# Performance work log

Hardware: AMD Instinct MI355X
Metric: run time of the kernel (lower is better)

## Reference

```python
import jax, jax.numpy as jnp
import numpy as np

LN_EPS = 1e-5


def setup_inputs() -> dict:
    key = jax.random.key(0)
    ks = jax.random.split(key, 10)
    b, n, m, d, e = 2, 4096, 32, 128, 64
    return {
        "t_ij": jax.random.normal(ks[0], (b, n, m, d), dtype=jnp.float32),
        "x1": jax.random.normal(ks[1], (b, n, d, 3), dtype=jnp.float32),
        "x2": jax.random.normal(ks[2], (b, n, d, 5), dtype=jnp.float32),
        "neighbor_indices": jax.random.randint(ks[3], (b, n, m), 0, n),
        "to_queries": jax.random.normal(ks[4], (d, e), dtype=jnp.float32),
        "to_keys1": jax.random.normal(ks[5], (d, e), dtype=jnp.float32),
        "to_keys2": jax.random.normal(ks[6], (d, e), dtype=jnp.float32),
        "ln_weight": jnp.ones((2 * e,), dtype=jnp.float32),
        "edge_w": jax.random.normal(ks[7], (2 * e, d), dtype=jnp.float32) / np.sqrt(2 * e),
        "res_w": jax.random.normal(ks[8], (d, d), dtype=jnp.float32) / np.sqrt(d),
    }


def _degree_inner_product(xl, to_queries, to_keys, neighbor_indices):
    # xl: [b n d ml]; projections over channel dim d -> e
    q = jnp.einsum('bndm,de->bnem', xl, to_queries)   # [b n e ml]
    k = jnp.einsum('bndm,de->bnem', xl, to_keys)      # [b n e ml]
    # gather neighbor keys: [b n j e ml]
    kg = jax.vmap(lambda kk, idx: kk[idx])(k, neighbor_indices)
    # inner product over multiplicity ml, per feature e: [b n j e]
    return jnp.einsum('bnem,bnjem->bnje', q, kg)


def reference(t_ij, x1, x2, neighbor_indices, to_queries, to_keys1, to_keys2,
              ln_weight, edge_w, res_w):
    ip1 = _degree_inner_product(x1, to_queries, to_keys1, neighbor_indices)
    ip2 = _degree_inner_product(x2, to_queries, to_keys2, neighbor_indices)
    w_ij = jnp.concatenate([ip1, ip2], axis=-1)  # [b n j 2e]
    # LayerNorm over last dim, weight only (bias=False)
    mu = jnp.mean(w_ij, axis=-1, keepdims=True)
    var = jnp.mean((w_ij - mu) ** 2, axis=-1, keepdims=True)
    w_ij = (w_ij - mu) * jax.lax.rsqrt(var + LN_EPS) * ln_weight
    edge_out = jax.nn.sigmoid(jnp.einsum('bnje,ed->bnjd', w_ij, edge_w))
    res_out = jnp.einsum('bnjd,de->bnje', t_ij, res_w)
    return edge_out + res_out
```

## Files before the change

kernel.cpp:

```cpp
#include <hip/hip_runtime.h>

#define B_ 2
#define N_ 4096
#define M_ 32
#define D_ 128
#define E_ 64
#define LN_EPS 1e-5f
#define WST 136
#define TOT (B_ * N_)

typedef __bf16 bf16x8 __attribute__((ext_vector_type(8)));
typedef float  f32x4  __attribute__((ext_vector_type(4)));

__global__ __launch_bounds__(256) void proj_kernel(
    const float* __restrict__ x1, const float* __restrict__ x2,
    const float* __restrict__ Wq, const float* __restrict__ Wk1,
    const float* __restrict__ Wk2,
    float* __restrict__ qws, __bf16* __restrict__ kws)
{
    __shared__ float xs[4][D_ * 8];
    const int lane = threadIdx.x & 63;
    const int wv   = threadIdx.x >> 6;
    const int bn   = blockIdx.x * 4 + wv;
    float* xw = xs[wv];
    const float* __restrict__ x1p = x1 + (size_t)bn * (D_ * 3);
    const float* __restrict__ x2p = x2 + (size_t)bn * (D_ * 5);
    for (int i = lane; i < D_ * 3; i += 64) xw[(i / 3) * 8 + (i % 3)]     = x1p[i];
    for (int i = lane; i < D_ * 5; i += 64) xw[(i / 5) * 8 + 3 + (i % 5)] = x2p[i];
    __syncthreads();

    float q[8] = {0.f,0.f,0.f,0.f,0.f,0.f,0.f,0.f};
    float k[8] = {0.f,0.f,0.f,0.f,0.f,0.f,0.f,0.f};
    #pragma unroll 4
    for (int d = 0; d < D_; ++d) {
        const float4 xa = *(const float4*)&xw[d * 8];
        const float4 xb = *(const float4*)&xw[d * 8 + 4];
        const float wq  = Wq [d * E_ + lane];
        const float wk1 = Wk1[d * E_ + lane];
        const float wk2 = Wk2[d * E_ + lane];
        q[0] += xa.x * wq;  q[1] += xa.y * wq;  q[2] += xa.z * wq;  q[3] += xa.w * wq;
        q[4] += xb.x * wq;  q[5] += xb.y * wq;  q[6] += xb.z * wq;  q[7] += xb.w * wq;
        k[0] += xa.x * wk1; k[1] += xa.y * wk1; k[2] += xa.z * wk1;
        k[3] += xa.w * wk2; k[4] += xb.x * wk2; k[5] += xb.y * wk2;
        k[6] += xb.z * wk2; k[7] += xb.w * wk2;
    }
    float4* qo = (float4*)(qws + ((size_t)bn * E_ + lane) * 8);
    qo[0] = make_float4(q[0], q[1], q[2], q[3]);
    qo[1] = make_float4(q[4], q[5], q[6], q[7]);
    bf16x8 kb;
    #pragma unroll
    for (int s = 0; s < 8; ++s) kb[s] = (__bf16)k[s];
    *(bf16x8*)(kws + ((size_t)bn * E_ + lane) * 8) = kb;
}

__global__ __launch_bounds__(256, 3) void fused_kernel(
    const float* __restrict__ t_ij, const int* __restrict__ nidx,
    const float* __restrict__ qws, const __bf16* __restrict__ kws,
    const float* __restrict__ ln_w,
    const float* __restrict__ edge_w, const float* __restrict__ res_w,
    float* __restrict__ out)
{
    __shared__ __bf16 wbuf[3][M_ * WST];

    const int t    = threadIdx.x;
    const int lane = t & 63;
    const int wvu  = t >> 6;
    const int r16  = lane & 15;
    const int quad = lane >> 4;
    const int n0   = wvu * 32;

    bf16x8 bE[2][4], bR[2][4];
    #pragma unroll
    for (int nt = 0; nt < 2; ++nt) {
        const int col = n0 + nt * 16 + r16;
        #pragma unroll
        for (int ks = 0; ks < 4; ++ks) {
            const int k0 = ks * 32 + quad * 8;
            bf16x8 fe, fr;
            #pragma unroll
            for (int j = 0; j < 8; ++j) {
                fe[j] = (__bf16)edge_w[(k0 + j) * D_ + col];
                fr[j] = (__bf16)res_w [(k0 + j) * D_ + col];
            }
            bE[nt][ks] = fe;
            bR[nt][ks] = fr;
        }
    }

    const float lnlo = ln_w[lane];
    const float lnhi = ln_w[64 + lane];

    auto phaseW = [&](int bn, __bf16* buf) {
        const int    b  = bn >> 12;
        const size_t jb = (size_t)bn * M_;
        const float* qp = qws + ((size_t)bn * E_ + lane) * 8;
        const float4 qa = *(const float4*)qp;
        const float4 qb = *(const float4*)(qp + 4);
        #pragma unroll 4
        for (int jj = 0; jj < 8; ++jj) {
            const int j  = wvu * 8 + jj;
            const int nj = nidx[jb + j];
            const bf16x8 kv =
                *(const bf16x8*)&kws[((size_t)(b * N_ + nj) * E_ + lane) * 8];
            const float wlo = qa.x * (float)kv[0] + qa.y * (float)kv[1]
                            + qa.z * (float)kv[2];
            const float whi = qa.w * (float)kv[3] + qb.x * (float)kv[4]
                            + qb.y * (float)kv[5] + qb.z * (float)kv[6]
                            + qb.w * (float)kv[7];
            float s1 = wlo + whi;
            float s2 = wlo * wlo + whi * whi;
            #pragma unroll
            for (int off = 1; off < 64; off <<= 1) {
                s1 += __shfl_xor(s1, off, 64);
                s2 += __shfl_xor(s2, off, 64);
            }
            const float mu  = s1 * (1.f / 128.f);
            const float var = fmaxf(s2 * (1.f / 128.f) - mu * mu, 0.f);
            const float rs  = rsqrtf(var + LN_EPS);
            buf[j * WST + lane]      = (__bf16)((wlo - mu) * rs * lnlo);
            buf[j * WST + 64 + lane] = (__bf16)((whi - mu) * rs * lnhi);
        }
    };

    auto tload = [&](int bn, bf16x8* tf) {
        const float* tp = t_ij + ((size_t)bn * M_ + r16) * D_;
        #pragma unroll
        for (int ks = 0; ks < 4; ++ks) {
            const int ko = ks * 32 + quad * 8;
            const float4 t0 = *(const float4*)(tp + ko);
            const float4 t1 = *(const float4*)(tp + ko + 4);
            bf16x8 a;
            a[0]=(__bf16)t0.x; a[1]=(__bf16)t0.y; a[2]=(__bf16)t0.z; a[3]=(__bf16)t0.w;
            a[4]=(__bf16)t1.x; a[5]=(__bf16)t1.y; a[6]=(__bf16)t1.z; a[7]=(__bf16)t1.w;
            tf[ks] = a;
        }
    };

    auto phaseM = [&](int bn, const __bf16* buf, const bf16x8* tf) {
        const size_t jb = (size_t)bn * M_;
        bf16x8 aT1[4];
        {
            const float* tp = t_ij + (jb + 16 + r16) * D_;
            #pragma unroll
            for (int ks = 0; ks < 4; ++ks) {
                const int ko = ks * 32 + quad * 8;
                const float4 t0 = *(const float4*)(tp + ko);
                const float4 t1 = *(const float4*)(tp + ko + 4);
                bf16x8 a;
                a[0]=(__bf16)t0.x; a[1]=(__bf16)t0.y; a[2]=(__bf16)t0.z; a[3]=(__bf16)t0.w;
                a[4]=(__bf16)t1.x; a[5]=(__bf16)t1.y; a[6]=(__bf16)t1.z; a[7]=(__bf16)t1.w;
                aT1[ks] = a;
            }
        }
        f32x4 accE[2][2], accR[2][2];
        #pragma unroll
        for (int mt = 0; mt < 2; ++mt)
            #pragma unroll
            for (int nt = 0; nt < 2; ++nt) {
                accE[mt][nt] = (f32x4){0.f,0.f,0.f,0.f};
                accR[mt][nt] = (f32x4){0.f,0.f,0.f,0.f};
            }
        #pragma unroll
        for (int ks = 0; ks < 4; ++ks) {
            const bf16x8 aW0 = *(const bf16x8*)&buf[r16 * WST + ks * 32 + quad * 8];
            const bf16x8 aW1 = *(const bf16x8*)&buf[(16 + r16) * WST + ks * 32 + quad * 8];
            #pragma unroll
            for (int nt = 0; nt < 2; ++nt) {
                accE[0][nt] = __builtin_amdgcn_mfma_f32_16x16x32_bf16(aW0,    bE[nt][ks], accE[0][nt], 0, 0, 0);
                accR[0][nt] = __builtin_amdgcn_mfma_f32_16x16x32_bf16(tf[ks], bR[nt][ks], accR[0][nt], 0, 0, 0);
                accE[1][nt] = __builtin_amdgcn_mfma_f32_16x16x32_bf16(aW1,    bE[nt][ks], accE[1][nt], 0, 0, 0);
                accR[1][nt] = __builtin_amdgcn_mfma_f32_16x16x32_bf16(aT1[ks],bR[nt][ks], accR[1][nt], 0, 0, 0);
            }
        }
        #pragma unroll
        for (int mt = 0; mt < 2; ++mt)
            #pragma unroll
            for (int nt = 0; nt < 2; ++nt)
                #pragma unroll
                for (int rr = 0; rr < 4; ++rr) {
                    const int row = mt * 16 + quad * 4 + rr;
                    const int col = n0 + nt * 16 + r16;
                    const float e  = accE[mt][nt][rr];
                    const float sg = 1.f / (1.f + __expf(-e));
                    out[(jb + row) * D_ + col] = sg + accR[mt][nt][rr];
                }
    };

    const int stride = gridDim.x;
    int bn = blockIdx.x;
    bf16x8 tf[4];
    phaseW(bn, wbuf[0]);
    tload(bn, tf);
    int buf = 0;
    for (; bn < TOT; bn += stride) {
        const int nb   = bn + stride;
        const int nbuf = (buf == 2) ? 0 : buf + 1;
        if (nb < TOT) phaseW(nb, wbuf[nbuf]);
        __syncthreads();
        phaseM(bn, wbuf[buf], tf);
        if (nb < TOT) tload(nb, tf);
        buf = nbuf;
    }
}

extern "C" void kernel_launch(void* const* d_in, const int* in_sizes, int n_in,
                              void* d_out, int out_size, void* d_ws, size_t ws_size,
                              hipStream_t stream) {
    const float* t_ij = (const float*)d_in[0];
    const float* x1   = (const float*)d_in[1];
    const float* x2   = (const float*)d_in[2];
    const int*   nidx = (const int*)  d_in[3];
    const float* Wq   = (const float*)d_in[4];
    const float* Wk1  = (const float*)d_in[5];
    const float* Wk2  = (const float*)d_in[6];
    const float* lnw  = (const float*)d_in[7];
    const float* eww  = (const float*)d_in[8];
    const float* rww  = (const float*)d_in[9];
    float* out = (float*)d_out;

    float*  qws = (float*)d_ws;
    __bf16* kws = (__bf16*)(qws + (size_t)TOT * E_ * 8);

    proj_kernel<<<TOT / 4, 256, 0, stream>>>(x1, x2, Wq, Wk1, Wk2, qws, kws);
    fused_kernel<<<768, 256, 0, stream>>>(t_ij, nidx, qws, kws, lnw, eww, rww, out);
}
```

Baseline: 383.0 us.

## Widen fused kernel to 8 waves and software-pipeline neighbor gathers two iterations ahead

The fused kernel now runs 512-thread blocks with 8 waves, each owning 16 output columns and 4 neighbor rows instead of 32 columns and 8 rows, on a grid of 512 blocks. Neighbor index loads are issued three iterations ahead and key gathers two ahead, held in registers, so gather latency overlaps the MFMA phase. Out-of-range prefetches are clamped to the last row instead of using branches. Each wave also loads both t_ij row tiles into registers one iteration early. This raises register pressure and adds redundant work at the tail of the loop.

```diff
diff --git a/kernel.cpp b/kernel.cpp
--- a/kernel.cpp
+++ b/kernel.cpp
@@ -8,6 +8,7 @@
 #define LN_EPS 1e-5f
 #define WST 136
 #define TOT (B_ * N_)
+#define FGRID 512
 
 typedef __bf16 bf16x8 __attribute__((ext_vector_type(8)));
 typedef float  f32x4  __attribute__((ext_vector_type(4)));
@@ -53,7 +54,7 @@
     *(bf16x8*)(kws + ((size_t)bn * E_ + lane) * 8) = kb;
 }
 
-__global__ __launch_bounds__(256, 3) void fused_kernel(
+__global__ __launch_bounds__(512, 4) void fused_kernel(
     const float* __restrict__ t_ij, const int* __restrict__ nidx,
     const float* __restrict__ qws, const __bf16* __restrict__ kws,
     const float* __restrict__ ln_w,
@@ -67,46 +68,56 @@
     const int wvu  = t >> 6;
     const int r16  = lane & 15;
     const int quad = lane >> 4;
-    const int n0   = wvu * 32;
-
-    bf16x8 bE[2][4], bR[2][4];
+    const int n0   = wvu * 16;
+
+    bf16x8 bE[4], bR[4];
     #pragma unroll
-    for (int nt = 0; nt < 2; ++nt) {
-        const int col = n0 + nt * 16 + r16;
-        #pragma unroll
-        for (int ks = 0; ks < 4; ++ks) {
-            const int k0 = ks * 32 + quad * 8;
-            bf16x8 fe, fr;
-            #pragma unroll
-            for (int j = 0; j < 8; ++j) {
-                fe[j] = (__bf16)edge_w[(k0 + j) * D_ + col];
-                fr[j] = (__bf16)res_w [(k0 + j) * D_ + col];
-            }
-            bE[nt][ks] = fe;
-            bR[nt][ks] = fr;
-        }
+    for (int ks = 0; ks < 4; ++ks) {
+        const int k0 = ks * 32 + quad * 8;
+        bf16x8 fe, fr;
+        #pragma unroll
+        for (int j = 0; j < 8; ++j) {
+            fe[j] = (__bf16)edge_w[(k0 + j) * D_ + n0 + r16];
+            fr[j] = (__bf16)res_w [(k0 + j) * D_ + n0 + r16];
+        }
+        bE[ks] = fe;
+        bR[ks] = fr;
     }
 
     const float lnlo = ln_w[lane];
     const float lnhi = ln_w[64 + lane];
-
-    auto phaseW = [&](int bn, __bf16* buf) {
-        const int    b  = bn >> 12;
-        const size_t jb = (size_t)bn * M_;
+    const int stride = gridDim.x;
+
+    int    ni[4];
+    bf16x8 kv[4];
+    float4 qa, qb;
+    bf16x8 tf[8];
+
+    auto nidxLoad = [&](int bn) {
+        const int* np = nidx + (size_t)bn * M_ + wvu * 4;
+        #pragma unroll
+        for (int jj = 0; jj < 4; ++jj) ni[jj] = np[jj];
+    };
+    auto gatherIssue = [&](int bn) {
+        const int b = bn >> 12;
+        #pragma unroll
+        for (int jj = 0; jj < 4; ++jj)
+            kv[jj] = *(const bf16x8*)&kws[((size_t)(b * N_ + ni[jj]) * E_ + lane) * 8];
         const float* qp = qws + ((size_t)bn * E_ + lane) * 8;
-        const float4 qa = *(const float4*)qp;
-        const float4 qb = *(const float4*)(qp + 4);
-        #pragma unroll 4
-        for (int jj = 0; jj < 8; ++jj) {
-            const int j  = wvu * 8 + jj;
-            const int nj = nidx[jb + j];
-            const bf16x8 kv =
-                *(const bf16x8*)&kws[((size_t)(b * N_ + nj) * E_ + lane) * 8];
-            const float wlo = qa.x * (float)kv[0] + qa.y * (float)kv[1]
-                            + qa.z * (float)kv[2];
-            const float whi = qa.w * (float)kv[3] + qb.x * (float)kv[4]
-                            + qb.y * (float)kv[5] + qb.z * (float)kv[6]
-                            + qb.w * (float)kv[7];
+        qa = *(const float4*)qp;
+        qb = *(const float4*)(qp + 4);
+    };
+
+    auto phaseW = [&](__bf16* buf) {
+        #pragma unroll
+        for (int jj = 0; jj < 4; ++jj) {
+            const int j = wvu * 4 + jj;
+            const bf16x8 k8 = kv[jj];
+            const float wlo = qa.x * (float)k8[0] + qa.y * (float)k8[1]
+                            + qa.z * (float)k8[2];
+            const float whi = qa.w * (float)k8[3] + qb.x * (float)k8[4]
+                            + qb.y * (float)k8[5] + qb.z * (float)k8[6]
+                            + qb.w * (float)k8[7];
             float s1 = wlo + whi;
             float s2 = wlo * wlo + whi * whi;
             #pragma unroll
@@ -122,83 +133,72 @@
         }
     };
 
-    auto tload = [&](int bn, bf16x8* tf) {
-        const float* tp = t_ij + ((size_t)bn * M_ + r16) * D_;
-        #pragma unroll
-        for (int ks = 0; ks < 4; ++ks) {
-            const int ko = ks * 32 + quad * 8;
-            const float4 t0 = *(const float4*)(tp + ko);
-            const float4 t1 = *(const float4*)(tp + ko + 4);
-            bf16x8 a;
-            a[0]=(__bf16)t0.x; a[1]=(__bf16)t0.y; a[2]=(__bf16)t0.z; a[3]=(__bf16)t0.w;
-            a[4]=(__bf16)t1.x; a[5]=(__bf16)t1.y; a[6]=(__bf16)t1.z; a[7]=(__bf16)t1.w;
-            tf[ks] = a;
-        }
-    };
-
-    auto phaseM = [&](int bn, const __bf16* buf, const bf16x8* tf) {
-        const size_t jb = (size_t)bn * M_;
-        bf16x8 aT1[4];
-        {
-            const float* tp = t_ij + (jb + 16 + r16) * D_;
+    auto tload = [&](int bn) {
+        const float* tp = t_ij + ((size_t)bn * M_) * D_;
+        #pragma unroll
+        for (int mt = 0; mt < 2; ++mt) {
+            const float* tpr = tp + (size_t)(mt * 16 + r16) * D_;
             #pragma unroll
             for (int ks = 0; ks < 4; ++ks) {
                 const int ko = ks * 32 + quad * 8;
-                const float4 t0 = *(const float4*)(tp + ko);
-                const float4 t1 = *(const float4*)(tp + ko + 4);
+                const float4 t0 = *(const float4*)(tpr + ko);
+                const float4 t1 = *(const float4*)(tpr + ko + 4);
                 bf16x8 a;
                 a[0]=(__bf16)t0.x; a[1]=(__bf16)t0.y; a[2]=(__bf16)t0.z; a[3]=(__bf16)t0.w;
                 a[4]=(__bf16)t1.x; a[5]=(__bf16)t1.y; a[6]=(__bf16)t1.z; a[7]=(__bf16)t1.w;
-                aT1[ks] = a;
+                tf[mt * 4 + ks] = a;
             }
         }
-        f32x4 accE[2][2], accR[2][2];
-        #pragma unroll
-        for (int mt = 0; mt < 2; ++mt)
-            #pragma unroll
-            for (int nt = 0; nt < 2; ++nt) {
-                accE[mt][nt] = (f32x4){0.f,0.f,0.f,0.f};
-                accR[mt][nt] = (f32x4){0.f,0.f,0.f,0.f};
-            }
+    };
+
+    auto phaseM = [&](int bn, const __bf16* buf) {
+        const size_t jb = (size_t)bn * M_;
+        f32x4 accE[2], accR[2];
+        #pragma unroll
+        for (int mt = 0; mt < 2; ++mt) {
+            accE[mt] = (f32x4){0.f,0.f,0.f,0.f};
+            accR[mt] = (f32x4){0.f,0.f,0.f,0.f};
+        }
         #pragma unroll
         for (int ks = 0; ks < 4; ++ks) {
             const bf16x8 aW0 = *(const bf16x8*)&buf[r16 * WST + ks * 32 + quad * 8];
             const bf16x8 aW1 = *(const bf16x8*)&buf[(16 + r16) * WST + ks * 32 + quad * 8];
-            #pragma unroll
-            for (int nt = 0; nt < 2; ++nt) {
-                accE[0][nt] = __builtin_amdgcn_mfma_f32_16x16x32_bf16(aW0,    bE[nt][ks], accE[0][nt], 0, 0, 0);
-                accR[0][nt] = __builtin_amdgcn_mfma_f32_16x16x32_bf16(tf[ks], bR[nt][ks], accR[0][nt], 0, 0, 0);
-                accE[1][nt] = __builtin_amdgcn_mfma_f32_16x16x32_bf16(aW1,    bE[nt][ks], accE[1][nt], 0, 0, 0);
-                accR[1][nt] = __builtin_amdgcn_mfma_f32_16x16x32_bf16(aT1[ks],bR[nt][ks], accR[1][nt], 0, 0, 0);
-            }
+            accE[0] = __builtin_amdgcn_mfma_f32_16x16x32_bf16(aW0,      bE[ks], accE[0], 0, 0, 0);
+            accR[0] = __builtin_amdgcn_mfma_f32_16x16x32_bf16(tf[ks],   bR[ks], accR[0], 0, 0, 0);
+            accE[1] = __builtin_amdgcn_mfma_f32_16x16x32_bf16(aW1,      bE[ks], accE[1], 0, 0, 0);
+            accR[1] = __builtin_amdgcn_mfma_f32_16x16x32_bf16(tf[4+ks], bR[ks], accR[1], 0, 0, 0);
         }
         #pragma unroll
         for (int mt = 0; mt < 2; ++mt)
             #pragma unroll
-            for (int nt = 0; nt < 2; ++nt)
-                #pragma unroll
-                for (int rr = 0; rr < 4; ++rr) {
-                    const int row = mt * 16 + quad * 4 + rr;
-                    const int col = n0 + nt * 16 + r16;
-                    const float e  = accE[mt][nt][rr];
-                    const float sg = 1.f / (1.f + __expf(-e));
-                    out[(jb + row) * D_ + col] = sg + accR[mt][nt][rr];
-                }
-    };
-
-    const int stride = gridDim.x;
-    int bn = blockIdx.x;
-    bf16x8 tf[4];
-    phaseW(bn, wbuf[0]);
-    tload(bn, tf);
+            for (int rr = 0; rr < 4; ++rr) {
+                const int row = mt * 16 + quad * 4 + rr;
+                const float e  = accE[mt][rr];
+                const float sg = 1.f / (1.f + __expf(-e));
+                out[(jb + row) * D_ + n0 + r16] = sg + accR[mt][rr];
+            }
+    };
+
+    const int bn0 = blockIdx.x;
+    auto cb = [](int x) { return x < TOT ? x : TOT - 1; };
+
+    nidxLoad(bn0);
+    gatherIssue(bn0);
+    nidxLoad(cb(bn0 + stride));
+    phaseW(wbuf[0]);
+    gatherIssue(cb(bn0 + stride));
+    nidxLoad(cb(bn0 + 2 * stride));
+    tload(bn0);
+
     int buf = 0;
-    for (; bn < TOT; bn += stride) {
-        const int nb   = bn + stride;
+    for (int bn = bn0; bn < TOT; bn += stride) {
         const int nbuf = (buf == 2) ? 0 : buf + 1;
-        if (nb < TOT) phaseW(nb, wbuf[nbuf]);
+        phaseW(wbuf[nbuf]);
         __syncthreads();
-        phaseM(bn, wbuf[buf], tf);
-        if (nb < TOT) tload(nb, tf);
+        phaseM(bn, wbuf[buf]);
+        gatherIssue(cb(bn + 2 * stride));
+        nidxLoad(cb(bn + 3 * stride));
+        tload(cb(bn + stride));
         buf = nbuf;
     }
 }
@@ -222,5 +222,5 @@
     __bf16* kws = (__bf16*)(qws + (size_t)TOT * E_ * 8);
 
     proj_kernel<<<TOT / 4, 256, 0, stream>>>(x1, x2, Wq, Wk1, Wk2, qws, kws);
-    fused_kernel<<<768, 256, 0, stream>>>(t_ij, nidx, qws, kws, lnw, eww, rww, out);
+    fused_kernel<<<FGRID, 512, 0, stream>>>(t_ij, nidx, qws, kws, lnw, eww, rww, out);
 }
```

Result: slower. 414.6 us (+8.2%).
